# Performance work log

Hardware: AMD Instinct MI355X
Metric: run time of the kernel (lower is better)

Reference implementation:

```python
import jax, jax.numpy as jnp
import numpy as np

INPUT, HIDDEN = 128, 64
B, T = 512, 1024


def _lstm_dir(x, Wih, Whh, b):
    """Single-direction LSTM (PyTorch gate order i,f,g,o). x: [B,T,I] -> [B,T,H]."""
    Bn = x.shape[0]
    H = Whh.shape[1]
    # precompute input contributions for all timesteps: [B,T,4H]
    xg = jnp.einsum('bti,gi->btg', x, Wih) + b

    def step(carry, g_t):
        h, c = carry
        g = g_t + h @ Whh.T  # [B,4H]
        i, f, gg, o = jnp.split(g, 4, axis=-1)
        c = jax.nn.sigmoid(f) * c + jax.nn.sigmoid(i) * jnp.tanh(gg)
        h = jax.nn.sigmoid(o) * jnp.tanh(c)
        return (h, c), h

    h0 = jnp.zeros((Bn, H), x.dtype)
    (_, _), hs = jax.lax.scan(step, (h0, h0), jnp.swapaxes(xg, 0, 1))
    return jnp.swapaxes(hs, 0, 1)  # [B,T,H]


def setup_inputs() -> dict:
    key = jax.random.key(0)
    ks = jax.random.split(key, 9)
    s_ih = 1.0 / np.sqrt(HIDDEN)
    def u(k, shape):
        return jax.random.uniform(k, shape, jnp.float32, -s_ih, s_ih)
    return {
        'x': jax.random.normal(ks[0], (B, T, INPUT), jnp.float32),
        'Wih_f': u(ks[1], (4 * HIDDEN, INPUT)),
        'Whh_f': u(ks[2], (4 * HIDDEN, HIDDEN)),
        'b_f': u(ks[3], (4 * HIDDEN,)),   # b_ih + b_hh folded (same math)
        'Wih_b': u(ks[4], (4 * HIDDEN, INPUT)),
        'Whh_b': u(ks[5], (4 * HIDDEN, HIDDEN)),
        'b_b': u(ks[6], (4 * HIDDEN,)),
    }


def reference(x, Wih_f, Whh_f, b_f, Wih_b, Whh_b, b_b):
    # forward returns the full bidirectional sequence output [B,T,2H]
    out_f = _lstm_dir(x, Wih_f, Whh_f, b_f)
    out_b = _lstm_dir(x[:, ::-1], Wih_b, Whh_b, b_b)[:, ::-1]
    return jnp.concatenate([out_f, out_b], axis=-1)
```

## Files before the change

kernel.cpp:

```cpp
#include <hip/hip_runtime.h>

#define T_LEN 1024
#define IN_DIM 128
#define HID 64
#define CH 8
#define NCH (T_LEN / CH)
#define XSTR 160
#define HSTR 96
#define OSTR 72

typedef __attribute__((ext_vector_type(8))) short short8;
typedef __attribute__((ext_vector_type(4))) float floatx4;
typedef __attribute__((ext_vector_type(2))) unsigned uintx2;

__device__ __forceinline__ unsigned short f2bf(float v) {
    union { float f; unsigned u; } a; a.f = v;
    unsigned r = a.u + 0x7FFFu + ((a.u >> 16) & 1u);
    return (unsigned short)(r >> 16);
}

__device__ __forceinline__ short8 cvt8(const float* p) {
    short8 r;
#pragma unroll
    for (int j = 0; j < 8; ++j) r[j] = (short)f2bf(p[j]);
    return r;
}

#define LOG2E 1.44269504088896f
__device__ __forceinline__ float sigm(float x) {
    return __builtin_amdgcn_rcpf(1.0f + __builtin_amdgcn_exp2f(x * -LOG2E));
}
__device__ __forceinline__ float tanh_(float x) {
    return 2.0f * __builtin_amdgcn_rcpf(1.0f + __builtin_amdgcn_exp2f(x * -2.0f * LOG2E)) - 1.0f;
}

__global__ __launch_bounds__(256, 1) void lstm_bidir(
    const float* __restrict__ x,
    const float* __restrict__ WihF, const float* __restrict__ WhhF, const float* __restrict__ bF,
    const float* __restrict__ WihB, const float* __restrict__ WhhB, const float* __restrict__ bB,
    float* __restrict__ out)
{
    const int tid  = threadIdx.x;
    const int w    = tid >> 6;
    const int lane = tid & 63;
    const int nloc = lane & 15;
    const int quad = lane >> 4;
    const int bid  = blockIdx.x;
    const int dir  = bid & 1;
    const int b0   = (bid >> 1) * 4;

    const float* Wih  = dir ? WihB : WihF;
    const float* Whh  = dir ? WhhB : WhhF;
    const float* bias = dir ? bB   : bF;

    __shared__ __align__(16) unsigned short xch[2][CH][4 * XSTR];
    __shared__ __align__(16) unsigned short h_s[2][4 * HSTR];
    __shared__ __align__(16) float obuf[2][CH][4][OSTR];

    for (int i = tid; i < 2 * 4 * HSTR; i += 256) ((unsigned short*)h_s)[i] = 0;

    short8 wihf[4][4];
    short8 whhf[4][2];
    float  bv[4];
#pragma unroll
    for (int gc = 0; gc < 4; ++gc) {
        const int row = gc * 64 + w * 16 + nloc;
        bv[gc] = bias[row];
#pragma unroll
        for (int kf = 0; kf < 4; ++kf)
            wihf[gc][kf] = cvt8(Wih + row * IN_DIM + kf * 32 + quad * 8);
#pragma unroll
        for (int kf = 0; kf < 2; ++kf)
            whhf[gc][kf] = cvt8(Whh + row * HID + kf * 32 + quad * 8);
    }

    auto tmap = [&](int s) {
        int ss = s < T_LEN - 1 ? s : T_LEN - 1;
        return dir ? (T_LEN - 1 - ss) : ss;
    };

    const int g   = tid >> 5;
    const int l32 = tid & 31;

#pragma unroll
    for (int i = 0; i < 4; ++i) {
        floatx4 v = *(const floatx4*)(x + (size_t)(b0 + i) * T_LEN * IN_DIM
                                        + (size_t)tmap(g) * IN_DIM + l32 * 4);
        unsigned lo = (unsigned)f2bf(v.x) | ((unsigned)f2bf(v.y) << 16);
        unsigned hi = (unsigned)f2bf(v.z) | ((unsigned)f2bf(v.w) << 16);
        uintx2 p = {lo, hi};
        *(uintx2*)&xch[0][g][i * XSTR + l32 * 4] = p;
    }

    float c = 0.f;

    __syncthreads();

    floatx4 xacc0[4], xacc1[4];
    {
        short8 xa[4];
        const unsigned short* xb = &xch[0][0][(nloc >> 2) * XSTR + quad * 8];
#pragma unroll
        for (int kf = 0; kf < 4; ++kf) xa[kf] = *(const short8*)(xb + kf * 32);
#pragma unroll
        for (int gc = 0; gc < 4; ++gc) xacc0[gc] = (floatx4){bv[gc], bv[gc], bv[gc], bv[gc]};
#pragma unroll
        for (int kf = 0; kf < 4; ++kf)
#pragma unroll
            for (int gc = 0; gc < 4; ++gc)
                xacc0[gc] = __builtin_amdgcn_mfma_f32_16x16x32_bf16(xa[kf], wihf[gc][kf], xacc0[gc], 0, 0, 0);
    }

    floatx4 stg[4];

    auto flushPrev = [&](int chkPrev) {
        const int pb  = chkPrev & 1;
        const int fs  = tid >> 5;
        const int fr  = (tid & 31) >> 3;
        const int fu  = (tid & 7) * 8;
        const float* src = &obuf[pb][fs][fr][fu];
        floatx4 v0 = *(const floatx4*)(src);
        floatx4 v1 = *(const floatx4*)(src + 4);
        const int tg = tmap(chkPrev * CH + fs);
        float* dst = out + ((size_t)(b0 + fr) * T_LEN + tg) * 128 + dir * HID + fu;
        *(floatx4*)(dst)     = v0;
        *(floatx4*)(dst + 4) = v1;
    };

    auto step = [&](int sl, int chk, int cbuf, floatx4* xaccC, floatx4* xaccN) {
        const int cur = sl & 1;

        if (sl == 0) {
            if (chk > 0) flushPrev(chk - 1);
            if (chk + 1 < NCH) {
                const int tn = (chk + 1) * CH + g;
#pragma unroll
                for (int i = 0; i < 4; ++i)
                    stg[i] = *(const floatx4*)(x + (size_t)(b0 + i) * T_LEN * IN_DIM
                                                 + (size_t)tmap(tn) * IN_DIM + l32 * 4);
            }
        }
        if (sl == 1 && chk + 1 < NCH) {
#pragma unroll
            for (int i = 0; i < 4; ++i) {
                unsigned lo = (unsigned)f2bf(stg[i].x) | ((unsigned)f2bf(stg[i].y) << 16);
                unsigned hi = (unsigned)f2bf(stg[i].z) | ((unsigned)f2bf(stg[i].w) << 16);
                uintx2 p = {lo, hi};
                *(uintx2*)&xch[cbuf ^ 1][g][i * XSTR + l32 * 4] = p;
            }
        }

        short8 ha[2];
        const unsigned short* hb = &h_s[cur][(nloc >> 2) * HSTR + quad * 8];
#pragma unroll
        for (int kf = 0; kf < 2; ++kf) ha[kf] = *(const short8*)(hb + kf * 32);

        short8 xa[4];
        const unsigned short* xb = (sl + 1 < CH)
            ? &xch[cbuf][sl + 1][(nloc >> 2) * XSTR + quad * 8]
            : &xch[cbuf ^ 1][0][(nloc >> 2) * XSTR + quad * 8];
#pragma unroll
        for (int kf = 0; kf < 4; ++kf) xa[kf] = *(const short8*)(xb + kf * 32);

        floatx4 acc[4];
#pragma unroll
        for (int gc = 0; gc < 4; ++gc)
            acc[gc] = __builtin_amdgcn_mfma_f32_16x16x32_bf16(ha[0], whhf[gc][0], xaccC[gc], 0, 0, 0);
#pragma unroll
        for (int gc = 0; gc < 4; ++gc)
            acc[gc] = __builtin_amdgcn_mfma_f32_16x16x32_bf16(ha[1], whhf[gc][1], acc[gc], 0, 0, 0);

#pragma unroll
        for (int gc = 0; gc < 4; ++gc) xaccN[gc] = (floatx4){bv[gc], bv[gc], bv[gc], bv[gc]};
#pragma unroll
        for (int kf = 0; kf < 4; ++kf)
#pragma unroll
            for (int gc = 0; gc < 4; ++gc)
                xaccN[gc] = __builtin_amdgcn_mfma_f32_16x16x32_bf16(xa[kf], wihf[gc][kf], xaccN[gc], 0, 0, 0);

        {
            float iv = sigm(acc[0][0]);
            float fv = sigm(acc[1][0]);
            float gv = tanh_(acc[2][0]);
            float ov = sigm(acc[3][0]);
            c = fv * c + iv * gv;
            float hv = ov * tanh_(c);
            obuf[cbuf][sl][quad][w * 16 + nloc] = hv;
            h_s[cur ^ 1][quad * HSTR + w * 16 + nloc] = f2bf(hv);
        }
        __syncthreads();
    };

    for (int chk = 0; chk < NCH; ++chk) {
        const int cbuf = chk & 1;
#pragma unroll
        for (int sp = 0; sp < CH; sp += 2) {
            step(sp,     chk, cbuf, xacc0, xacc1);
            step(sp + 1, chk, cbuf, xacc1, xacc0);
        }
    }
    flushPrev(NCH - 1);
}

extern "C" void kernel_launch(void* const* d_in, const int* in_sizes, int n_in,
                              void* d_out, int out_size, void* d_ws, size_t ws_size,
                              hipStream_t stream) {
    const float* x    = (const float*)d_in[0];
    const float* WihF = (const float*)d_in[1];
    const float* WhhF = (const float*)d_in[2];
    const float* bF   = (const float*)d_in[3];
    const float* WihB = (const float*)d_in[4];
    const float* WhhB = (const float*)d_in[5];
    const float* bB   = (const float*)d_in[6];
    float* out = (float*)d_out;

    lstm_bidir<<<dim3(256), dim3(256), 0, stream>>>(x, WihF, WhhF, bF, WihB, WhhB, bB, out);
}
```

Baseline: 775.1 us.

## Halve batch rows per block to launch twice as many blocks

Each block now processes 2 batch rows instead of 4, so the grid doubles to 512 blocks and launch bounds allow 2 blocks per CU. The MFMA A-operand mapping changes so lanes index rows via nloc>>3, and only half the quads write h and output. The goal is more parallelism across the 256 CUs and more latency hiding for the serial recurrence. In exchange, half of each MFMA's work is redundant and the weights are loaded and converted by twice as many blocks.

```diff
diff --git a/kernel.cpp b/kernel.cpp
--- a/kernel.cpp
+++ b/kernel.cpp
@@ -5,13 +5,13 @@
 #define HID 64
 #define CH 8
 #define NCH (T_LEN / CH)
+#define ROWS 2
 #define XSTR 160
 #define HSTR 96
 #define OSTR 72
 
 typedef __attribute__((ext_vector_type(8))) short short8;
 typedef __attribute__((ext_vector_type(4))) float floatx4;
-typedef __attribute__((ext_vector_type(2))) unsigned uintx2;
 
 __device__ __forceinline__ unsigned short f2bf(float v) {
     union { float f; unsigned u; } a; a.f = v;
@@ -26,6 +26,15 @@
     return r;
 }
 
+__device__ __forceinline__ short8 pack8(floatx4 a, floatx4 b) {
+    short8 r;
+    r[0] = (short)f2bf(a.x); r[1] = (short)f2bf(a.y);
+    r[2] = (short)f2bf(a.z); r[3] = (short)f2bf(a.w);
+    r[4] = (short)f2bf(b.x); r[5] = (short)f2bf(b.y);
+    r[6] = (short)f2bf(b.z); r[7] = (short)f2bf(b.w);
+    return r;
+}
+
 #define LOG2E 1.44269504088896f
 __device__ __forceinline__ float sigm(float x) {
     return __builtin_amdgcn_rcpf(1.0f + __builtin_amdgcn_exp2f(x * -LOG2E));
@@ -34,7 +43,7 @@
     return 2.0f * __builtin_amdgcn_rcpf(1.0f + __builtin_amdgcn_exp2f(x * -2.0f * LOG2E)) - 1.0f;
 }
 
-__global__ __launch_bounds__(256, 1) void lstm_bidir(
+__global__ __launch_bounds__(256, 2) void lstm_bidir(
     const float* __restrict__ x,
     const float* __restrict__ WihF, const float* __restrict__ WhhF, const float* __restrict__ bF,
     const float* __restrict__ WihB, const float* __restrict__ WhhB, const float* __restrict__ bB,
@@ -45,19 +54,20 @@
     const int lane = tid & 63;
     const int nloc = lane & 15;
     const int quad = lane >> 4;
+    const int brow = quad >> 1;
     const int bid  = blockIdx.x;
     const int dir  = bid & 1;
-    const int b0   = (bid >> 1) * 4;
+    const int b0   = (bid >> 1) * ROWS;
 
     const float* Wih  = dir ? WihB : WihF;
     const float* Whh  = dir ? WhhB : WhhF;
     const float* bias = dir ? bB   : bF;
 
-    __shared__ __align__(16) unsigned short xch[2][CH][4 * XSTR];
-    __shared__ __align__(16) unsigned short h_s[2][4 * HSTR];
-    __shared__ __align__(16) float obuf[2][CH][4][OSTR];
-
-    for (int i = tid; i < 2 * 4 * HSTR; i += 256) ((unsigned short*)h_s)[i] = 0;
+    __shared__ __align__(16) unsigned short xch[2][CH][ROWS * XSTR];
+    __shared__ __align__(16) unsigned short h_s[2][ROWS * HSTR];
+    __shared__ __align__(16) float obuf[2][CH][ROWS][OSTR];
+
+    for (int i = tid; i < 2 * ROWS * HSTR; i += 256) ((unsigned short*)h_s)[i] = 0;
 
     short8 wihf[4][4];
     short8 whhf[4][2];
@@ -79,17 +89,17 @@
         return dir ? (T_LEN - 1 - ss) : ss;
     };
 
-    const int g   = tid >> 5;
-    const int l32 = tid & 31;
-
-#pragma unroll
-    for (int i = 0; i < 4; ++i) {
-        floatx4 v = *(const floatx4*)(x + (size_t)(b0 + i) * T_LEN * IN_DIM
-                                        + (size_t)tmap(g) * IN_DIM + l32 * 4);
-        unsigned lo = (unsigned)f2bf(v.x) | ((unsigned)f2bf(v.y) << 16);
-        unsigned hi = (unsigned)f2bf(v.z) | ((unsigned)f2bf(v.w) << 16);
-        uintx2 p = {lo, hi};
-        *(uintx2*)&xch[0][g][i * XSTR + l32 * 4] = p;
+    const int g    = tid >> 5;
+    const int l32  = tid & 31;
+    const int srow = l32 >> 4;
+    const int sc8  = (l32 & 15) * 8;
+    const float* xrow = x + (size_t)(b0 + srow) * T_LEN * IN_DIM + sc8;
+
+    {
+        const float* p = xrow + (size_t)tmap(g) * IN_DIM;
+        floatx4 v0 = *(const floatx4*)(p);
+        floatx4 v1 = *(const floatx4*)(p + 4);
+        *(short8*)&xch[0][g][srow * XSTR + sc8] = pack8(v0, v1);
     }
 
     float c = 0.f;
@@ -99,7 +109,7 @@
     floatx4 xacc0[4], xacc1[4];
     {
         short8 xa[4];
-        const unsigned short* xb = &xch[0][0][(nloc >> 2) * XSTR + quad * 8];
+        const unsigned short* xb = &xch[0][0][(nloc >> 3) * XSTR + quad * 8];
 #pragma unroll
         for (int kf = 0; kf < 4; ++kf) xa[kf] = *(const short8*)(xb + kf * 32);
 #pragma unroll
@@ -111,20 +121,16 @@
                 xacc0[gc] = __builtin_amdgcn_mfma_f32_16x16x32_bf16(xa[kf], wihf[gc][kf], xacc0[gc], 0, 0, 0);
     }
 
-    floatx4 stg[4];
+    floatx4 stg[2];
 
     auto flushPrev = [&](int chkPrev) {
-        const int pb  = chkPrev & 1;
-        const int fs  = tid >> 5;
-        const int fr  = (tid & 31) >> 3;
-        const int fu  = (tid & 7) * 8;
-        const float* src = &obuf[pb][fs][fr][fu];
-        floatx4 v0 = *(const floatx4*)(src);
-        floatx4 v1 = *(const floatx4*)(src + 4);
+        const int pb = chkPrev & 1;
+        const int fs = tid >> 5;
+        const int fr = (tid >> 4) & 1;
+        const int fu = (tid & 15) * 4;
+        floatx4 v = *(const floatx4*)&obuf[pb][fs][fr][fu];
         const int tg = tmap(chkPrev * CH + fs);
-        float* dst = out + ((size_t)(b0 + fr) * T_LEN + tg) * 128 + dir * HID + fu;
-        *(floatx4*)(dst)     = v0;
-        *(floatx4*)(dst + 4) = v1;
+        *(floatx4*)(out + ((size_t)(b0 + fr) * T_LEN + tg) * 128 + dir * HID + fu) = v;
     };
 
     auto step = [&](int sl, int chk, int cbuf, floatx4* xaccC, floatx4* xaccN) {
@@ -133,32 +139,23 @@
         if (sl == 0) {
             if (chk > 0) flushPrev(chk - 1);
             if (chk + 1 < NCH) {
-                const int tn = (chk + 1) * CH + g;
-#pragma unroll
-                for (int i = 0; i < 4; ++i)
-                    stg[i] = *(const floatx4*)(x + (size_t)(b0 + i) * T_LEN * IN_DIM
-                                                 + (size_t)tmap(tn) * IN_DIM + l32 * 4);
+                const float* p = xrow + (size_t)tmap((chk + 1) * CH + g) * IN_DIM;
+                stg[0] = *(const floatx4*)(p);
+                stg[1] = *(const floatx4*)(p + 4);
             }
         }
-        if (sl == 1 && chk + 1 < NCH) {
-#pragma unroll
-            for (int i = 0; i < 4; ++i) {
-                unsigned lo = (unsigned)f2bf(stg[i].x) | ((unsigned)f2bf(stg[i].y) << 16);
-                unsigned hi = (unsigned)f2bf(stg[i].z) | ((unsigned)f2bf(stg[i].w) << 16);
-                uintx2 p = {lo, hi};
-                *(uintx2*)&xch[cbuf ^ 1][g][i * XSTR + l32 * 4] = p;
-            }
-        }
+        if (sl == 1 && chk + 1 < NCH)
+            *(short8*)&xch[cbuf ^ 1][g][srow * XSTR + sc8] = pack8(stg[0], stg[1]);
 
         short8 ha[2];
-        const unsigned short* hb = &h_s[cur][(nloc >> 2) * HSTR + quad * 8];
+        const unsigned short* hb = &h_s[cur][(nloc >> 3) * HSTR + quad * 8];
 #pragma unroll
         for (int kf = 0; kf < 2; ++kf) ha[kf] = *(const short8*)(hb + kf * 32);
 
         short8 xa[4];
         const unsigned short* xb = (sl + 1 < CH)
-            ? &xch[cbuf][sl + 1][(nloc >> 2) * XSTR + quad * 8]
-            : &xch[cbuf ^ 1][0][(nloc >> 2) * XSTR + quad * 8];
+            ? &xch[cbuf][sl + 1][(nloc >> 3) * XSTR + quad * 8]
+            : &xch[cbuf ^ 1][0][(nloc >> 3) * XSTR + quad * 8];
 #pragma unroll
         for (int kf = 0; kf < 4; ++kf) xa[kf] = *(const short8*)(xb + kf * 32);
 
@@ -185,8 +182,10 @@
             float ov = sigm(acc[3][0]);
             c = fv * c + iv * gv;
             float hv = ov * tanh_(c);
-            obuf[cbuf][sl][quad][w * 16 + nloc] = hv;
-            h_s[cur ^ 1][quad * HSTR + w * 16 + nloc] = f2bf(hv);
+            if ((quad & 1) == 0) {
+                obuf[cbuf][sl][brow][w * 16 + nloc] = hv;
+                h_s[cur ^ 1][brow * HSTR + w * 16 + nloc] = f2bf(hv);
+            }
         }
         __syncthreads();
     };
@@ -214,5 +213,5 @@
     const float* bB   = (const float*)d_in[6];
     float* out = (float*)d_out;
 
-    lstm_bidir<<<dim3(256), dim3(256), 0, stream>>>(x, WihF, WhhF, bF, WihB, WhhB, bB, out);
-}
+    lstm_bidir<<<dim3(512), dim3(256), 0, stream>>>(x, WihF, WhhF, bF, WihB, WhhB, bB, out);
+}
```

Result: slower. 887.0 us (+14.4%).

## Batch input projection over four timesteps and spread MFMAs across steps

Applied to the files above, without the earlier changes.

Instead of 16 input-projection MFMAs per timestep using only 4 of the 16 M rows, the kernel packs 4 timesteps × 4 batch rows into the full 16-row MFMA tile and computes it over four steps, one K-slice per step. That is 4 MFMAs per step instead of 16. Each step pulls its precomputed gate preactivations out of the packed tile with ds_bpermute and lane selects, and uses them to seed the recurrent accumulators. This cuts matrix-core work on the serial critical path, at the cost of 16 cross-lane permutes per step and more complex indexing.

```diff
diff --git a/kernel.cpp b/kernel.cpp
--- a/kernel.cpp
+++ b/kernel.cpp
@@ -25,6 +25,9 @@
     for (int j = 0; j < 8; ++j) r[j] = (short)f2bf(p[j]);
     return r;
 }
+
+__device__ __forceinline__ float i2f(int v) { union { int i; float f; } u; u.i = v; return u.f; }
+__device__ __forceinline__ int   f2i(float v) { union { float f; int i; } u; u.f = v; return u.i; }
 
 #define LOG2E 1.44269504088896f
 __device__ __forceinline__ float sigm(float x) {
@@ -93,22 +96,20 @@
     }
 
     float c = 0.f;
+    const bool q1 = (quad & 1) != 0;
+    const bool q2 = (quad & 2) != 0;
 
     __syncthreads();
 
-    floatx4 xacc0[4], xacc1[4];
-    {
-        short8 xa[4];
-        const unsigned short* xb = &xch[0][0][(nloc >> 2) * XSTR + quad * 8];
-#pragma unroll
-        for (int kf = 0; kf < 4; ++kf) xa[kf] = *(const short8*)(xb + kf * 32);
-#pragma unroll
-        for (int gc = 0; gc < 4; ++gc) xacc0[gc] = (floatx4){bv[gc], bv[gc], bv[gc], bv[gc]};
-#pragma unroll
-        for (int kf = 0; kf < 4; ++kf)
-#pragma unroll
-            for (int gc = 0; gc < 4; ++gc)
-                xacc0[gc] = __builtin_amdgcn_mfma_f32_16x16x32_bf16(xa[kf], wihf[gc][kf], xacc0[gc], 0, 0, 0);
+    floatx4 TBA[4], TBB[4];
+#pragma unroll
+    for (int gc = 0; gc < 4; ++gc) TBA[gc] = (floatx4){bv[gc], bv[gc], bv[gc], bv[gc]};
+#pragma unroll
+    for (int kf = 0; kf < 4; ++kf) {
+        short8 xa = *(const short8*)&xch[0][nloc >> 2][(nloc & 3) * XSTR + kf * 32 + quad * 8];
+#pragma unroll
+        for (int gc = 0; gc < 4; ++gc)
+            TBA[gc] = __builtin_amdgcn_mfma_f32_16x16x32_bf16(xa, wihf[gc][kf], TBA[gc], 0, 0, 0);
     }
 
     floatx4 stg[4];
@@ -127,8 +128,9 @@
         *(floatx4*)(dst + 4) = v1;
     };
 
-    auto step = [&](int sl, int chk, int cbuf, floatx4* xaccC, floatx4* xaccN) {
-        const int cur = sl & 1;
+    auto stepT = [&](int sl, int chk, int cbuf, floatx4* TBuse, floatx4* TBbuild) {
+        const int cur  = sl & 1;
+        const int tloc = sl & 3;
 
         if (sl == 0) {
             if (chk > 0) flushPrev(chk - 1);
@@ -150,33 +152,50 @@
             }
         }
 
+        float xg[4];
+        {
+            const int addr = (tloc * 16 + nloc) * 4;
+#pragma unroll
+            for (int gc = 0; gc < 4; ++gc) {
+                float f0 = i2f(__builtin_amdgcn_ds_bpermute(addr, f2i(TBuse[gc][0])));
+                float f1 = i2f(__builtin_amdgcn_ds_bpermute(addr, f2i(TBuse[gc][1])));
+                float f2 = i2f(__builtin_amdgcn_ds_bpermute(addr, f2i(TBuse[gc][2])));
+                float f3 = i2f(__builtin_amdgcn_ds_bpermute(addr, f2i(TBuse[gc][3])));
+                float a  = q1 ? f1 : f0;
+                float b_ = q1 ? f3 : f2;
+                xg[gc] = q2 ? b_ : a;
+            }
+        }
+
         short8 ha[2];
         const unsigned short* hb = &h_s[cur][(nloc >> 2) * HSTR + quad * 8];
 #pragma unroll
         for (int kf = 0; kf < 2; ++kf) ha[kf] = *(const short8*)(hb + kf * 32);
 
-        short8 xa[4];
-        const unsigned short* xb = (sl + 1 < CH)
-            ? &xch[cbuf][sl + 1][(nloc >> 2) * XSTR + quad * 8]
-            : &xch[cbuf ^ 1][0][(nloc >> 2) * XSTR + quad * 8];
-#pragma unroll
-        for (int kf = 0; kf < 4; ++kf) xa[kf] = *(const short8*)(xb + kf * 32);
-
         floatx4 acc[4];
 #pragma unroll
+        for (int gc = 0; gc < 4; ++gc) acc[gc] = (floatx4){xg[gc], xg[gc], xg[gc], xg[gc]};
+#pragma unroll
         for (int gc = 0; gc < 4; ++gc)
-            acc[gc] = __builtin_amdgcn_mfma_f32_16x16x32_bf16(ha[0], whhf[gc][0], xaccC[gc], 0, 0, 0);
+            acc[gc] = __builtin_amdgcn_mfma_f32_16x16x32_bf16(ha[0], whhf[gc][0], acc[gc], 0, 0, 0);
 #pragma unroll
         for (int gc = 0; gc < 4; ++gc)
             acc[gc] = __builtin_amdgcn_mfma_f32_16x16x32_bf16(ha[1], whhf[gc][1], acc[gc], 0, 0, 0);
 
-#pragma unroll
-        for (int gc = 0; gc < 4; ++gc) xaccN[gc] = (floatx4){bv[gc], bv[gc], bv[gc], bv[gc]};
-#pragma unroll
-        for (int kf = 0; kf < 4; ++kf)
+        {
+            const unsigned short* xb = (sl < 4)
+                ? &xch[cbuf][4 + (nloc >> 2)][(nloc & 3) * XSTR + tloc * 32 + quad * 8]
+                : &xch[cbuf ^ 1][nloc >> 2][(nloc & 3) * XSTR + tloc * 32 + quad * 8];
+            short8 xa = *(const short8*)xb;
+            if (tloc == 0) {
+#pragma unroll
+                for (int gc = 0; gc < 4; ++gc)
+                    TBbuild[gc] = (floatx4){bv[gc], bv[gc], bv[gc], bv[gc]};
+            }
 #pragma unroll
             for (int gc = 0; gc < 4; ++gc)
-                xaccN[gc] = __builtin_amdgcn_mfma_f32_16x16x32_bf16(xa[kf], wihf[gc][kf], xaccN[gc], 0, 0, 0);
+                TBbuild[gc] = __builtin_amdgcn_mfma_f32_16x16x32_bf16(xa, wihf[gc][tloc], TBbuild[gc], 0, 0, 0);
+        }
 
         {
             float iv = sigm(acc[0][0]);
@@ -194,9 +213,9 @@
     for (int chk = 0; chk < NCH; ++chk) {
         const int cbuf = chk & 1;
 #pragma unroll
-        for (int sp = 0; sp < CH; sp += 2) {
-            step(sp,     chk, cbuf, xacc0, xacc1);
-            step(sp + 1, chk, cbuf, xacc1, xacc0);
+        for (int sl = 0; sl < CH; ++sl) {
+            if (sl < 4) stepT(sl, chk, cbuf, TBA, TBB);
+            else        stepT(sl, chk, cbuf, TBB, TBA);
         }
     }
     flushPrev(NCH - 1);
```

Result: slower. 872.8 us (+12.6%).
